# Kernel tuning notes

Hardware: AMD Instinct MI355X
Metric: run time of the kernel (lower is better)

## Reference

```python
import jax, jax.numpy as jnp
import numpy as np
from jax import lax

WINDOW = 9
N_INT = 1000
WMSE_WEIGHTS = np.array([1.0, 2.0, 5.0, 10.0, 30.0], dtype=np.float32)
WMSE_THRESH = np.array([0.5, 2.0, 5.0, 10.0], dtype=np.float32)
LOSS_W = np.array([1e-4, 1.0], dtype=np.float32)


def setup_inputs() -> dict:
    key = jax.random.key(0)
    k1, k2 = jax.random.split(key)
    shape = (4, 1, 128, 128)
    return {
        "prediction": jax.random.normal(k1, shape, dtype=jnp.float32),
        "target": jax.random.normal(k2, shape, dtype=jnp.float32),
    }


def _box_mean(x, win):
    # Equivalent to the original shift-and-accumulate running mean: box sum over
    # in-bounds neighbors (edge-corrected mean). x: [B, 1, H, W].
    pad = win // 2
    k = jnp.ones((1, 1, win, win), x.dtype)
    num = lax.conv_general_dilated(x, k, (1, 1), [(pad, pad), (pad, pad)])
    ones = jnp.ones((1, 1) + x.shape[-2:], x.dtype)
    den = lax.conv_general_dilated(ones, k, (1, 1), [(pad, pad), (pad, pad)])
    return num / den


def _wmse(pred, tgt):
    # Threshold-weighted MSE: weight chosen by the largest threshold <= target.
    w = jnp.full_like(tgt, WMSE_WEIGHTS[0])
    for i in range(len(WMSE_THRESH)):
        w = jnp.where(tgt >= WMSE_THRESH[i], WMSE_WEIGHTS[i + 1], w)
    return jnp.mean(w * (pred - tgt) ** 2)


def _crps(pred, tgt, n):
    # Deterministic CRPS via numeric integration over n points spanning the
    # global data range: integral (H(x - pred) - H(x - tgt))^2 dx per pixel.
    lo = jnp.minimum(pred.min(), tgt.min())
    hi = jnp.maximum(pred.max(), tgt.max())
    x = jnp.linspace(lo, hi, n)
    dx = (hi - lo) / (n - 1)
    p = pred.reshape(-1)
    t = tgt.reshape(-1)
    Fp = x[:, None] >= p[None, :]  # [N_INT, n_pixels]
    Ft = x[:, None] >= t[None, :]
    sq = (Fp ^ Ft).astype(pred.dtype)  # (Fp - Ft)^2 for 0/1 indicators
    return jnp.mean(sq.sum(axis=0) * dx)


def reference(prediction, target):
    pred_dist = prediction - _box_mean(prediction, WINDOW)
    tgt_dist = target - _box_mean(target, WINDOW)
    wmse = _wmse(prediction, target)
    crps = _crps(pred_dist, tgt_dist, N_INT)
    return LOSS_W[0] * wmse + LOSS_W[1] * crps
```

## Files before the change

### kernel.cpp

```cpp
#include <hip/hip_runtime.h>

#define NBLK 256
#define NTHR 256

__device__ __forceinline__ void compute_dists(const float* __restrict__ pred,
                                              const float* __restrict__ tgt,
                                              int idx, float& pv, float& tv,
                                              float& pd, float& td) {
    int b   = idx >> 14;
    int rem = idx & 16383;
    int i   = rem >> 7;
    int j   = rem & 127;
    const float* p = pred + (b << 14);
    const float* t = tgt  + (b << 14);
    float sp = 0.f, st = 0.f;
#pragma unroll
    for (int di = -4; di <= 4; ++di) {
        int ii = i + di;
        if ((unsigned)ii >= 128u) continue;
        int base = ii << 7;
#pragma unroll
        for (int dj = -4; dj <= 4; ++dj) {
            int jj = j + dj;
            if ((unsigned)jj >= 128u) continue;
            sp += p[base + jj];
            st += t[base + jj];
        }
    }
    int rc = min(i, 4) + min(127 - i, 4) + 1;
    int cc = min(j, 4) + min(127 - j, 4) + 1;
    float den = (float)(rc * cc);
    pv = p[(i << 7) + j];
    tv = t[(i << 7) + j];
    pd = pv - sp / den;
    td = tv - st / den;
}

__global__ void SPL_k1(const float* __restrict__ pred, const float* __restrict__ tgt,
                       float* __restrict__ part) {
    int idx = blockIdx.x * NTHR + threadIdx.x;
    float pv, tv, pd, td;
    compute_dists(pred, tgt, idx, pv, tv, pd, td);

    float w = 1.f;
    if (tv >= 0.5f) w = 2.f;
    if (tv >= 2.f)  w = 5.f;
    if (tv >= 5.f)  w = 10.f;
    if (tv >= 10.f) w = 30.f;
    float d  = pv - tv;
    float s  = w * d * d;
    float mn = fminf(pd, td);
    float mx = fmaxf(pd, td);

    for (int o = 32; o > 0; o >>= 1) {
        s  += __shfl_down(s, o, 64);
        mn  = fminf(mn, __shfl_down(mn, o, 64));
        mx  = fmaxf(mx, __shfl_down(mx, o, 64));
    }
    __shared__ float ss[4], smn[4], smx[4];
    int lane = threadIdx.x & 63, wid = threadIdx.x >> 6;
    if (lane == 0) { ss[wid] = s; smn[wid] = mn; smx[wid] = mx; }
    __syncthreads();
    if (threadIdx.x == 0) {
        part[blockIdx.x]            = ss[0] + ss[1] + ss[2] + ss[3];
        part[NBLK + blockIdx.x]     = fminf(fminf(smn[0], smn[1]), fminf(smn[2], smn[3]));
        part[2 * NBLK + blockIdx.x] = fmaxf(fmaxf(smx[0], smx[1]), fmaxf(smx[2], smx[3]));
    }
}

__global__ void SPL_k2(const float* __restrict__ part, float* __restrict__ scal) {
    int tid = threadIdx.x;
    float s  = part[tid];
    float mn = part[NBLK + tid];
    float mx = part[2 * NBLK + tid];
    for (int o = 32; o > 0; o >>= 1) {
        s  += __shfl_down(s, o, 64);
        mn  = fminf(mn, __shfl_down(mn, o, 64));
        mx  = fmaxf(mx, __shfl_down(mx, o, 64));
    }
    __shared__ float ss[4], smn[4], smx[4];
    int lane = tid & 63, wid = tid >> 6;
    if (lane == 0) { ss[wid] = s; smn[wid] = mn; smx[wid] = mx; }
    __syncthreads();
    if (tid == 0) {
        scal[0] = fminf(fminf(smn[0], smn[1]), fminf(smn[2], smn[3]));
        scal[1] = fmaxf(fmaxf(smx[0], smx[1]), fmaxf(smx[2], smx[3]));
        scal[2] = ss[0] + ss[1] + ss[2] + ss[3];
    }
}

__global__ void SPL_k3(const float* __restrict__ pred, const float* __restrict__ tgt,
                       const float* __restrict__ scal, int* __restrict__ cpart) {
    int idx = blockIdx.x * NTHR + threadIdx.x;
    float pv, tv, pd, td;
    compute_dists(pred, tgt, idx, pv, tv, pd, td);

    float lo = scal[0], hi = scal[1];
    float dx = (hi - lo) / 999.0f;
    float a  = fminf(pd, td);
    float b  = fmaxf(pd, td);
    int ka = (int)ceilf((a - lo) / dx);
    int kb = (int)ceilf((b - lo) / dx);
    if (ka < 0) ka = 0;
    if (kb > 1000) kb = 1000;
    int cnt = kb - ka;
    if (cnt < 0) cnt = 0;

    for (int o = 32; o > 0; o >>= 1) cnt += __shfl_down(cnt, o, 64);
    __shared__ int sc[4];
    int lane = threadIdx.x & 63, wid = threadIdx.x >> 6;
    if (lane == 0) sc[wid] = cnt;
    __syncthreads();
    if (threadIdx.x == 0) cpart[blockIdx.x] = sc[0] + sc[1] + sc[2] + sc[3];
}

__global__ void SPL_k4(const int* __restrict__ cpart, const float* __restrict__ scal,
                       float* __restrict__ out) {
    int tid = threadIdx.x;
    int c = cpart[tid];
    for (int o = 32; o > 0; o >>= 1) c += __shfl_down(c, o, 64);
    __shared__ int sc[4];
    int lane = tid & 63, wid = tid >> 6;
    if (lane == 0) sc[wid] = c;
    __syncthreads();
    if (tid == 0) {
        long long total = (long long)sc[0] + sc[1] + sc[2] + sc[3];
        float lo = scal[0], hi = scal[1];
        float dx = (hi - lo) / 999.0f;
        float wmse = scal[2] * (1.0f / 65536.0f);
        double crps = (double)total * (double)dx / 65536.0;
        out[0] = 1e-4f * wmse + (float)crps;
    }
}

extern "C" void kernel_launch(void* const* d_in, const int* in_sizes, int n_in,
                              void* d_out, int out_size, void* d_ws, size_t ws_size,
                              hipStream_t stream) {
    const float* pred = (const float*)d_in[0];
    const float* tgt  = (const float*)d_in[1];
    float* part  = (float*)d_ws;
    float* scal  = part + 3 * NBLK;
    int*   cpart = (int*)(scal + 4);
    float* out   = (float*)d_out;

    SPL_k1<<<NBLK, NTHR, 0, stream>>>(pred, tgt, part);
    SPL_k2<<<1, NBLK, 0, stream>>>(part, scal);
    SPL_k3<<<NBLK, NTHR, 0, stream>>>(pred, tgt, scal, cpart);
    SPL_k4<<<1, NBLK, 0, stream>>>(cpart, scal, out);
}
```

Before: 77.65 us.

## Fuse four kernels into two using LDS separable box filter and stored distances

The first kernel now stages a 10-row halo tile in shared memory and computes the 9x9 box mean separably (vertical then horizontal sums). It writes the per-pixel distance pairs to a workspace buffer so they need not be recomputed. A single 1024-thread block then reduces the partials and counts the CRPS bins over the stored distances, replacing three kernels. This removes two launches and the redundant stencil pass, but the CRPS counting now runs on only one workgroup.

```diff
diff --git a/kernel.cpp b/kernel.cpp
--- a/kernel.cpp
+++ b/kernel.cpp
@@ -1,46 +1,64 @@
 #include <hip/hip_runtime.h>
 
-#define NBLK 256
-#define NTHR 256
 
-__device__ __forceinline__ void compute_dists(const float* __restrict__ pred,
+__global__ __launch_bounds__(256) void SPL_kA(const float* __restrict__ pred,
                                               const float* __restrict__ tgt,
-                                              int idx, float& pv, float& tv,
-                                              float& pd, float& td) {
-    int b   = idx >> 14;
-    int rem = idx & 16383;
-    int i   = rem >> 7;
-    int j   = rem & 127;
-    const float* p = pred + (b << 14);
-    const float* t = tgt  + (b << 14);
+                                              float* __restrict__ part,
+                                              float2* __restrict__ dist) {
+    __shared__ float sP[1280], sT[1280];
+    __shared__ float vsP[256], vsT[256];
+    __shared__ float red[12];
+
+    int b = blockIdx.x;
+    int t = threadIdx.x;
+    int m  = b >> 6;
+    int r2 = (b & 63) << 1;
+    const float* p = pred + (m << 14);
+    const float* q = tgt  + (m << 14);
+
+#pragma unroll
+    for (int s = 0; s < 5; ++s) {
+        int k   = t + s * 256;
+        int rr  = k >> 7;
+        int cc  = k & 127;
+        int grw = r2 - 4 + rr;
+        bool ok = (unsigned)grw < 128u;
+        sP[k] = ok ? p[(grw << 7) + cc] : 0.f;
+        sT[k] = ok ? q[(grw << 7) + cc] : 0.f;
+    }
+    __syncthreads();
+
+    int orow = t >> 7;
+    int col  = t & 127;
+    int row  = r2 + orow;
+
+    float vp = 0.f, vt = 0.f;
+    int vb = orow * 128 + col;
+#pragma unroll
+    for (int di = 0; di < 9; ++di) {
+        vp += sP[vb + di * 128];
+        vt += sT[vb + di * 128];
+    }
+    vsP[t] = vp; vsT[t] = vt;
+    __syncthreads();
+
     float sp = 0.f, st = 0.f;
+    int rbase = t & ~127;
 #pragma unroll
-    for (int di = -4; di <= 4; ++di) {
-        int ii = i + di;
-        if ((unsigned)ii >= 128u) continue;
-        int base = ii << 7;
-#pragma unroll
-        for (int dj = -4; dj <= 4; ++dj) {
-            int jj = j + dj;
-            if ((unsigned)jj >= 128u) continue;
-            sp += p[base + jj];
-            st += t[base + jj];
-        }
+    for (int dj = -4; dj <= 4; ++dj) {
+        int jj = col + dj;
+        if ((unsigned)jj < 128u) { sp += vsP[rbase + jj]; st += vsT[rbase + jj]; }
     }
-    int rc = min(i, 4) + min(127 - i, 4) + 1;
-    int cc = min(j, 4) + min(127 - j, 4) + 1;
-    float den = (float)(rc * cc);
-    pv = p[(i << 7) + j];
-    tv = t[(i << 7) + j];
-    pd = pv - sp / den;
-    td = tv - st / den;
-}
 
-__global__ void SPL_k1(const float* __restrict__ pred, const float* __restrict__ tgt,
-                       float* __restrict__ part) {
-    int idx = blockIdx.x * NTHR + threadIdx.x;
-    float pv, tv, pd, td;
-    compute_dists(pred, tgt, idx, pv, tv, pd, td);
+    int   rc  = min(row, 4) + min(127 - row, 4) + 1;
+    int   cn  = min(col, 4) + min(127 - col, 4) + 1;
+    float den = (float)(rc * cn);
+    float pv  = sP[(orow + 4) * 128 + col];
+    float tv  = sT[(orow + 4) * 128 + col];
+    float pd  = pv - sp / den;
+    float td  = tv - st / den;
+
+    dist[(b << 8) + t] = make_float2(pd, td);
 
     float w = 1.f;
     if (tv >= 0.5f) w = 2.f;
@@ -57,78 +75,68 @@
         mn  = fminf(mn, __shfl_down(mn, o, 64));
         mx  = fmaxf(mx, __shfl_down(mx, o, 64));
     }
-    __shared__ float ss[4], smn[4], smx[4];
-    int lane = threadIdx.x & 63, wid = threadIdx.x >> 6;
-    if (lane == 0) { ss[wid] = s; smn[wid] = mn; smx[wid] = mx; }
+    int lane = t & 63, wid = t >> 6;
+    if (lane == 0) { red[wid] = s; red[4 + wid] = mn; red[8 + wid] = mx; }
     __syncthreads();
-    if (threadIdx.x == 0) {
-        part[blockIdx.x]            = ss[0] + ss[1] + ss[2] + ss[3];
-        part[NBLK + blockIdx.x]     = fminf(fminf(smn[0], smn[1]), fminf(smn[2], smn[3]));
-        part[2 * NBLK + blockIdx.x] = fmaxf(fmaxf(smx[0], smx[1]), fmaxf(smx[2], smx[3]));
+    if (t == 0) {
+        part[b]       = red[0] + red[1] + red[2] + red[3];
+        part[256 + b] = fminf(fminf(red[4], red[5]), fminf(red[6], red[7]));
+        part[512 + b] = fmaxf(fmaxf(red[8], red[9]), fmaxf(red[10], red[11]));
     }
 }
 
-__global__ void SPL_k2(const float* __restrict__ part, float* __restrict__ scal) {
-    int tid = threadIdx.x;
-    float s  = part[tid];
-    float mn = part[NBLK + tid];
-    float mx = part[2 * NBLK + tid];
+__global__ __launch_bounds__(1024) void SPL_kB(const float* __restrict__ part,
+                                               const float2* __restrict__ dist,
+                                               float* __restrict__ out) {
+    __shared__ float rs[16], rmn[16], rmx[16];
+    __shared__ int   rci[16];
+    __shared__ float bc[3];
+
+    int t = threadIdx.x;
+    int lane = t & 63, wid = t >> 6;
+
+    float s = 0.f, mn = 3.4e38f, mx = -3.4e38f;
+    if (t < 256) { s = part[t]; mn = part[256 + t]; mx = part[512 + t]; }
     for (int o = 32; o > 0; o >>= 1) {
         s  += __shfl_down(s, o, 64);
         mn  = fminf(mn, __shfl_down(mn, o, 64));
         mx  = fmaxf(mx, __shfl_down(mx, o, 64));
     }
-    __shared__ float ss[4], smn[4], smx[4];
-    int lane = tid & 63, wid = tid >> 6;
-    if (lane == 0) { ss[wid] = s; smn[wid] = mn; smx[wid] = mx; }
+    if (lane == 0) { rs[wid] = s; rmn[wid] = mn; rmx[wid] = mx; }
     __syncthreads();
-    if (tid == 0) {
-        scal[0] = fminf(fminf(smn[0], smn[1]), fminf(smn[2], smn[3]));
-        scal[1] = fmaxf(fmaxf(smx[0], smx[1]), fmaxf(smx[2], smx[3]));
-        scal[2] = ss[0] + ss[1] + ss[2] + ss[3];
+    if (t == 0) {
+        float ss = 0.f, m1 = 3.4e38f, m2 = -3.4e38f;
+        for (int i = 0; i < 16; ++i) {
+            ss += rs[i]; m1 = fminf(m1, rmn[i]); m2 = fmaxf(m2, rmx[i]);
+        }
+        bc[0] = m1; bc[1] = m2; bc[2] = ss;
     }
-}
+    __syncthreads();
 
-__global__ void SPL_k3(const float* __restrict__ pred, const float* __restrict__ tgt,
-                       const float* __restrict__ scal, int* __restrict__ cpart) {
-    int idx = blockIdx.x * NTHR + threadIdx.x;
-    float pv, tv, pd, td;
-    compute_dists(pred, tgt, idx, pv, tv, pd, td);
+    float lo = bc[0], hi = bc[1];
+    float dx = (hi - lo) / 999.0f;
 
-    float lo = scal[0], hi = scal[1];
-    float dx = (hi - lo) / 999.0f;
-    float a  = fminf(pd, td);
-    float b  = fmaxf(pd, td);
-    int ka = (int)ceilf((a - lo) / dx);
-    int kb = (int)ceilf((b - lo) / dx);
-    if (ka < 0) ka = 0;
-    if (kb > 1000) kb = 1000;
-    int cnt = kb - ka;
-    if (cnt < 0) cnt = 0;
-
+    int cnt = 0;
+#pragma unroll 4
+    for (int it = 0; it < 64; ++it) {
+        float2 d = dist[it * 1024 + t];
+        float a  = fminf(d.x, d.y);
+        float b2 = fmaxf(d.x, d.y);
+        int ka = (int)ceilf((a - lo) / dx);
+        int kb = (int)ceilf((b2 - lo) / dx);
+        if (ka < 0) ka = 0;
+        if (kb > 1000) kb = 1000;
+        int c = kb - ka;
+        if (c > 0) cnt += c;
+    }
     for (int o = 32; o > 0; o >>= 1) cnt += __shfl_down(cnt, o, 64);
-    __shared__ int sc[4];
-    int lane = threadIdx.x & 63, wid = threadIdx.x >> 6;
-    if (lane == 0) sc[wid] = cnt;
+    if (lane == 0) rci[wid] = cnt;
     __syncthreads();
-    if (threadIdx.x == 0) cpart[blockIdx.x] = sc[0] + sc[1] + sc[2] + sc[3];
-}
-
-__global__ void SPL_k4(const int* __restrict__ cpart, const float* __restrict__ scal,
-                       float* __restrict__ out) {
-    int tid = threadIdx.x;
-    int c = cpart[tid];
-    for (int o = 32; o > 0; o >>= 1) c += __shfl_down(c, o, 64);
-    __shared__ int sc[4];
-    int lane = tid & 63, wid = tid >> 6;
-    if (lane == 0) sc[wid] = c;
-    __syncthreads();
-    if (tid == 0) {
-        long long total = (long long)sc[0] + sc[1] + sc[2] + sc[3];
-        float lo = scal[0], hi = scal[1];
-        float dx = (hi - lo) / 999.0f;
-        float wmse = scal[2] * (1.0f / 65536.0f);
-        double crps = (double)total * (double)dx / 65536.0;
+    if (t == 0) {
+        long long tot = 0;
+        for (int i = 0; i < 16; ++i) tot += rci[i];
+        float  wmse = bc[2] * (1.0f / 65536.0f);
+        double crps = (double)tot * (double)dx / 65536.0;
         out[0] = 1e-4f * wmse + (float)crps;
     }
 }
@@ -138,13 +146,10 @@
                               hipStream_t stream) {
     const float* pred = (const float*)d_in[0];
     const float* tgt  = (const float*)d_in[1];
-    float* part  = (float*)d_ws;
-    float* scal  = part + 3 * NBLK;
-    int*   cpart = (int*)(scal + 4);
-    float* out   = (float*)d_out;
+    float*  part = (float*)d_ws;
+    float2* dist = (float2*)(part + 768);
+    float*  out  = (float*)d_out;
 
-    SPL_k1<<<NBLK, NTHR, 0, stream>>>(pred, tgt, part);
-    SPL_k2<<<1, NBLK, 0, stream>>>(part, scal);
-    SPL_k3<<<NBLK, NTHR, 0, stream>>>(pred, tgt, scal, cpart);
-    SPL_k4<<<1, NBLK, 0, stream>>>(cpart, scal, out);
+    SPL_kA<<<256, 256, 0, stream>>>(pred, tgt, part, dist);
+    SPL_kB<<<1, 1024, 0, stream>>>(part, dist, out);
 }
```

New measurement: 76.97 us. No clear change (-0.9%).
